# Performance work log

Measured on AMD Instinct MI355X. Metric: run time of the kernel, lower is better.

The kernel has to match this reference:

```python
import jax, jax.numpy as jnp
import numpy as np

N_NODES = 100000
N_EDGES = 1600000
IN_DIM, HID_DIM, OUT_DIM = 128, 64, 32


def gcn_conv(x, edge_index, W, b, n_nodes):
    """PyG GCNConv: add self-loops, symmetric deg^-1/2 normalization,
    linear transform, gather->scatter-sum aggregation, then bias."""
    loops = jnp.arange(n_nodes, dtype=edge_index.dtype)
    src = jnp.concatenate([edge_index[0], loops])  # [E+N]
    dst = jnp.concatenate([edge_index[1], loops])  # [E+N]
    # degree over targets (includes self-loops)
    deg = jax.ops.segment_sum(jnp.ones_like(dst, dtype=x.dtype), dst,
                              num_segments=n_nodes)
    dinv = jnp.where(deg > 0, jax.lax.rsqrt(deg), 0.0)
    norm = dinv[src] * dinv[dst]                   # [E+N]
    h = x @ W                                      # [N, F_out]
    msg = h[src] * norm[:, None]                   # gather + scale
    out = jax.ops.segment_sum(msg, dst, num_segments=n_nodes)
    return out + b


def setup_inputs() -> dict:
    key = jax.random.key(0)
    k1, k2, k3, k4 = jax.random.split(key, 4)
    x = jax.random.normal(k1, (N_NODES, IN_DIM), dtype=jnp.float32)
    edge_index = jax.random.randint(k2, (2, N_EDGES), 0, N_NODES,
                                    dtype=jnp.int64)
    # Glorot-ish init for weights, zero bias (PyG default: glorot + zeros)
    W1 = jax.random.normal(k3, (IN_DIM, HID_DIM), dtype=jnp.float32) * (1.0 / np.sqrt(IN_DIM))
    b1 = jnp.zeros((HID_DIM,), dtype=jnp.float32)
    W2 = jax.random.normal(k4, (HID_DIM, OUT_DIM), dtype=jnp.float32) * (1.0 / np.sqrt(HID_DIM))
    b2 = jnp.zeros((OUT_DIM,), dtype=jnp.float32)
    return {"x": x, "edge_index": edge_index, "W1": W1, "b1": b1,
            "W2": W2, "b2": b2}


def reference(x, edge_index, W1, b1, W2, b2):
    n = x.shape[0]
    h = jax.nn.relu(gcn_conv(x, edge_index, W1, b1, n))
    return gcn_conv(h, edge_index, W2, b2, n)
```

## Files before the change

kernel.cpp:

```cpp
#include <hip/hip_runtime.h>


#define BLK 256
#define BLKC 1024
#define EPT 8
#define BSHIFT 10
#define NPB 1024
#define SLOTB 18432
#define NBMAX 128

typedef unsigned int uint_t;
typedef unsigned short ushort_t;
typedef __attribute__((ext_vector_type(2))) float v2f;
typedef __attribute__((ext_vector_type(8))) short bf16x8;
typedef __attribute__((ext_vector_type(4))) float f32x4;

__device__ __forceinline__ uint_t f2bf(float x) {
    union { float f; uint_t u; } un; un.f = x;
    uint_t u = un.u;
    return (u + 0x7fffu + ((u >> 16) & 1u)) >> 16;
}

__device__ __forceinline__ void pkadd(v2f& a0, v2f& a1, v2f& a2, v2f& a3, uint4 v) {
    v2f p;
    p.x = __uint_as_float(v.x << 16); p.y = __uint_as_float(v.x & 0xffff0000u); a0 += p;
    p.x = __uint_as_float(v.y << 16); p.y = __uint_as_float(v.y & 0xffff0000u); a1 += p;
    p.x = __uint_as_float(v.z << 16); p.y = __uint_as_float(v.z & 0xffff0000u); a2 += p;
    p.x = __uint_as_float(v.w << 16); p.y = __uint_as_float(v.w & 0xffff0000u); a3 += p;
}

__device__ __forceinline__ bool detect64(const int* __restrict__ idx) {
    int z = 0;
#pragma unroll
    for (int i = 1; i < 32; i += 2) z |= idx[i];
    return z == 0;
}

__global__ void k_part(const int* __restrict__ idx, int* __restrict__ bcursor,
                       int* __restrict__ edge_part, int E, int nbuck) {
    __shared__ int h[NBMAX];
    __shared__ int rb[NBMAX];
    bool is64 = detect64(idx);
    int t = threadIdx.x, blk = blockIdx.x;
    for (int i = t; i < nbuck; i += BLK) h[i] = 0;
    __syncthreads();
    int base = blk * (BLK * EPT) + t;
    int dst[EPT], src[EPT];
#pragma unroll
    for (int k = 0; k < EPT; ++k) {
        int e = base + k * BLK;
        if (e < E) {
            if (is64) {
                uint2 dv = ((const uint2*)idx)[(size_t)E + e];
                uint2 sv = ((const uint2*)idx)[e];
                dst[k] = (int)dv.x;
                src[k] = (int)sv.x;
            } else {
                dst[k] = idx[E + e];
                src[k] = idx[e];
            }
            atomicAdd(&h[dst[k] >> BSHIFT], 1);
        } else {
            dst[k] = -1;
        }
    }
    __syncthreads();
    for (int i = t; i < nbuck; i += BLK) {
        int c = h[i];
        rb[i] = c ? atomicAdd(&bcursor[i], c) : 0;
        h[i] = 0;
    }
    __syncthreads();
#pragma unroll
    for (int k = 0; k < EPT; ++k) {
        if (dst[k] >= 0) {
            int b = dst[k] >> BSHIFT;
            int r = atomicAdd(&h[b], 1);
            edge_part[(size_t)b * SLOTB + rb[b] + r] =
                src[k] | ((dst[k] & (NPB - 1)) << 17);
        }
    }
}

__global__ __launch_bounds__(BLKC) void k_csr(
        const int* __restrict__ edge_part, const int* __restrict__ bcursor,
        int* __restrict__ row_ptr, int* __restrict__ deg, float* __restrict__ dinv,
        int* __restrict__ csr_src, int N, int nbuck) {
    __shared__ int cnt[NPB];
    __shared__ int off[NPB];
    int b = blockIdx.x, t = threadIdx.x;
    int node0 = b << BSHIFT;
    int nn = min(NPB, N - node0);
    int m = bcursor[b];
    size_t ebase = (size_t)b * SLOTB;
    cnt[t] = 0;
    __syncthreads();
    for (int e = t; e < m; e += BLKC)
        atomicAdd(&cnt[((unsigned)edge_part[ebase + e]) >> 17], 1);
    __syncthreads();
    off[t] = cnt[t];
    __syncthreads();
    for (int st = 1; st < BLKC; st <<= 1) {
        int v = (t >= st) ? off[t - st] : 0;
        __syncthreads();
        off[t] += v;
        __syncthreads();
    }
    int excl = off[t] - cnt[t];
    off[t] = excl;
    if (t < nn) {
        row_ptr[node0 + t] = (int)(ebase + excl);
        deg[node0 + t] = cnt[t];
        dinv[node0 + t] = rsqrtf((float)(cnt[t] + 1));
    }
    __syncthreads();
    for (int e = t; e < m; e += BLKC) {
        int p = edge_part[ebase + e];
        int dlo = ((unsigned)p) >> 17;
        int r = atomicAdd(&off[dlo], 1);
        csr_src[ebase + r] = p & 0x1FFFF;
    }
}

__global__ __launch_bounds__(256) void k_gemm1(
        const float* __restrict__ x, const float* __restrict__ W1,
        const float* __restrict__ dinv, ushort_t* __restrict__ hs1, int N) {
    __shared__ ushort_t xb[64][136];
    __shared__ ushort_t wb[64][136];
    int t = threadIdx.x;
    int rbase = blockIdx.x * 64;
    for (int i = t; i < 2048; i += BLK) {
        int k = i >> 4, n4 = i & 15;
        float4 w = ((const float4*)W1)[i];
        wb[4 * n4 + 0][k] = (ushort_t)f2bf(w.x);
        wb[4 * n4 + 1][k] = (ushort_t)f2bf(w.y);
        wb[4 * n4 + 2][k] = (ushort_t)f2bf(w.z);
        wb[4 * n4 + 3][k] = (ushort_t)f2bf(w.w);
    }
    for (int i = t; i < 2048; i += BLK) {
        int r = i >> 5, c4 = i & 31;
        int rr = rbase + r; if (rr >= N) rr = N - 1;
        float4 v = ((const float4*)x)[(size_t)rr * 32 + c4];
        uint2 p;
        p.x = f2bf(v.x) | (f2bf(v.y) << 16);
        p.y = f2bf(v.z) | (f2bf(v.w) << 16);
        *(uint2*)&xb[r][4 * c4] = p;
    }
    __syncthreads();
    int w = t >> 6, l = t & 63;
    int lane16 = l & 15, quad = l >> 4;
    int mrow = 16 * w + lane16;
    f32x4 acc0 = {0.f, 0.f, 0.f, 0.f}, acc1 = {0.f, 0.f, 0.f, 0.f};
    f32x4 acc2 = {0.f, 0.f, 0.f, 0.f}, acc3 = {0.f, 0.f, 0.f, 0.f};
#pragma unroll
    for (int kk = 0; kk < 4; ++kk) {
        int k0 = kk * 32 + quad * 8;
        bf16x8 a  = *(const bf16x8*)&xb[mrow][k0];
        bf16x8 b0 = *(const bf16x8*)&wb[lane16][k0];
        bf16x8 b1 = *(const bf16x8*)&wb[lane16 + 16][k0];
        bf16x8 b2 = *(const bf16x8*)&wb[lane16 + 32][k0];
        bf16x8 b3 = *(const bf16x8*)&wb[lane16 + 48][k0];
        acc0 = __builtin_amdgcn_mfma_f32_16x16x32_bf16(a, b0, acc0, 0, 0, 0);
        acc1 = __builtin_amdgcn_mfma_f32_16x16x32_bf16(a, b1, acc1, 0, 0, 0);
        acc2 = __builtin_amdgcn_mfma_f32_16x16x32_bf16(a, b2, acc2, 0, 0, 0);
        acc3 = __builtin_amdgcn_mfma_f32_16x16x32_bf16(a, b3, acc3, 0, 0, 0);
    }
    __syncthreads();
    int orow = 16 * w + quad * 4;
    float d0 = dinv[min(rbase + orow + 0, N - 1)];
    float d1 = dinv[min(rbase + orow + 1, N - 1)];
    float d2 = dinv[min(rbase + orow + 2, N - 1)];
    float d3 = dinv[min(rbase + orow + 3, N - 1)];
    xb[orow + 0][lane16]      = (ushort_t)f2bf(acc0.x * d0);
    xb[orow + 1][lane16]      = (ushort_t)f2bf(acc0.y * d1);
    xb[orow + 2][lane16]      = (ushort_t)f2bf(acc0.z * d2);
    xb[orow + 3][lane16]      = (ushort_t)f2bf(acc0.w * d3);
    xb[orow + 0][lane16 + 16] = (ushort_t)f2bf(acc1.x * d0);
    xb[orow + 1][lane16 + 16] = (ushort_t)f2bf(acc1.y * d1);
    xb[orow + 2][lane16 + 16] = (ushort_t)f2bf(acc1.z * d2);
    xb[orow + 3][lane16 + 16] = (ushort_t)f2bf(acc1.w * d3);
    xb[orow + 0][lane16 + 32] = (ushort_t)f2bf(acc2.x * d0);
    xb[orow + 1][lane16 + 32] = (ushort_t)f2bf(acc2.y * d1);
    xb[orow + 2][lane16 + 32] = (ushort_t)f2bf(acc2.z * d2);
    xb[orow + 3][lane16 + 32] = (ushort_t)f2bf(acc2.w * d3);
    xb[orow + 0][lane16 + 48] = (ushort_t)f2bf(acc3.x * d0);
    xb[orow + 1][lane16 + 48] = (ushort_t)f2bf(acc3.y * d1);
    xb[orow + 2][lane16 + 48] = (ushort_t)f2bf(acc3.z * d2);
    xb[orow + 3][lane16 + 48] = (ushort_t)f2bf(acc3.w * d3);
    __syncthreads();
    for (int i = t; i < 512; i += BLK) {
        int r = i >> 3, c8 = i & 7;
        int rr = rbase + r;
        if (rr < N) {
            uint4 v = *(const uint4*)&xb[r][8 * c8];
            *(uint4*)&hs1[(size_t)rr * 64 + 8 * c8] = v;
        }
    }
}

__global__ void k_agg1(const uint_t* __restrict__ hs1, const int* __restrict__ row_ptr,
                       const int* __restrict__ deg, const int* __restrict__ csr_src,
                       const float* __restrict__ dinv, const float* __restrict__ b1,
                       ushort_t* __restrict__ a1b, int N) {
    int lane = threadIdx.x & 63;
    int g = lane >> 3;
    int c = lane & 7;
    int wavebase = ((blockIdx.x * blockDim.x + threadIdx.x) >> 6) * 8;
    int node = wavebase + g;
    bool alive = node < N;
    int nodeC = alive ? node : N - 1;
    const uint4* H = (const uint4*)hs1;
    v2f a0 = {0.f, 0.f}, a1_ = {0.f, 0.f}, a2 = {0.f, 0.f}, a3 = {0.f, 0.f};
    float dn = dinv[nodeC];
    int beg = row_ptr[nodeC];
    int tot = alive ? deg[nodeC] : 0;
    pkadd(a0, a1_, a2, a3, H[(size_t)nodeC * 8 + c]);
    int gbase = lane & 0x38;
    for (int eb = 0; __any(eb < tot); eb += 8) {
        int jal = 0;
        if (eb + c < tot) jal = csr_src[beg + eb + c];
        int cnt = tot - eb;
        uint4 vv[8];
#pragma unroll
        for (int e = 0; e < 8; ++e) {
            int j = __shfl(jal, gbase + e, 64);
            if (e < cnt) vv[e] = H[(size_t)j * 8 + c];
        }
#pragma unroll
        for (int e = 0; e < 8; ++e) {
            if (e < cnt) pkadd(a0, a1_, a2, a3, vv[e]);
        }
    }
    if (alive) {
        const float4* B = (const float4*)b1;
        float4 bv0 = B[2 * c], bv1 = B[2 * c + 1];
        float o0 = fmaxf(fmaf(a0.x, dn, bv0.x), 0.f);
        float o1 = fmaxf(fmaf(a0.y, dn, bv0.y), 0.f);
        float o2 = fmaxf(fmaf(a1_.x, dn, bv0.z), 0.f);
        float o3 = fmaxf(fmaf(a1_.y, dn, bv0.w), 0.f);
        float o4 = fmaxf(fmaf(a2.x, dn, bv1.x), 0.f);
        float o5 = fmaxf(fmaf(a2.y, dn, bv1.y), 0.f);
        float o6 = fmaxf(fmaf(a3.x, dn, bv1.z), 0.f);
        float o7 = fmaxf(fmaf(a3.y, dn, bv1.w), 0.f);
        uint4 o;
        o.x = f2bf(o0) | (f2bf(o1) << 16);
        o.y = f2bf(o2) | (f2bf(o3) << 16);
        o.z = f2bf(o4) | (f2bf(o5) << 16);
        o.w = f2bf(o6) | (f2bf(o7) << 16);
        ((uint4*)a1b)[(size_t)node * 8 + c] = o;
    }
}

__global__ __launch_bounds__(256) void k_gemm2(
        const ushort_t* __restrict__ a1b, const float* __restrict__ W2,
        const float* __restrict__ dinv, ushort_t* __restrict__ hs2, int N) {
    __shared__ ushort_t ab[64][72];
    __shared__ ushort_t wb[32][72];
    int t = threadIdx.x;
    int rbase = blockIdx.x * 64;
    for (int i = t; i < 512; i += BLK) {
        int k = i >> 3, n4 = i & 7;
        float4 w = ((const float4*)W2)[i];
        wb[4 * n4 + 0][k] = (ushort_t)f2bf(w.x);
        wb[4 * n4 + 1][k] = (ushort_t)f2bf(w.y);
        wb[4 * n4 + 2][k] = (ushort_t)f2bf(w.z);
        wb[4 * n4 + 3][k] = (ushort_t)f2bf(w.w);
    }
    for (int i = t; i < 512; i += BLK) {
        int r = i >> 3, c8 = i & 7;
        int rr = rbase + r; if (rr >= N) rr = N - 1;
        uint4 v = ((const uint4*)a1b)[(size_t)rr * 8 + c8];
        *(uint4*)&ab[r][8 * c8] = v;
    }
    __syncthreads();
    int w = t >> 6, l = t & 63;
    int lane16 = l & 15, quad = l >> 4;
    int mrow = 16 * w + lane16;
    f32x4 acc0 = {0.f, 0.f, 0.f, 0.f}, acc1 = {0.f, 0.f, 0.f, 0.f};
#pragma unroll
    for (int kk = 0; kk < 2; ++kk) {
        int k0 = kk * 32 + quad * 8;
        bf16x8 a  = *(const bf16x8*)&ab[mrow][k0];
        bf16x8 b0 = *(const bf16x8*)&wb[lane16][k0];
        bf16x8 b1 = *(const bf16x8*)&wb[lane16 + 16][k0];
        acc0 = __builtin_amdgcn_mfma_f32_16x16x32_bf16(a, b0, acc0, 0, 0, 0);
        acc1 = __builtin_amdgcn_mfma_f32_16x16x32_bf16(a, b1, acc1, 0, 0, 0);
    }
    __syncthreads();
    int orow = 16 * w + quad * 4;
    float d0 = dinv[min(rbase + orow + 0, N - 1)];
    float d1 = dinv[min(rbase + orow + 1, N - 1)];
    float d2 = dinv[min(rbase + orow + 2, N - 1)];
    float d3 = dinv[min(rbase + orow + 3, N - 1)];
    ab[orow + 0][lane16]      = (ushort_t)f2bf(acc0.x * d0);
    ab[orow + 1][lane16]      = (ushort_t)f2bf(acc0.y * d1);
    ab[orow + 2][lane16]      = (ushort_t)f2bf(acc0.z * d2);
    ab[orow + 3][lane16]      = (ushort_t)f2bf(acc0.w * d3);
    ab[orow + 0][lane16 + 16] = (ushort_t)f2bf(acc1.x * d0);
    ab[orow + 1][lane16 + 16] = (ushort_t)f2bf(acc1.y * d1);
    ab[orow + 2][lane16 + 16] = (ushort_t)f2bf(acc1.z * d2);
    ab[orow + 3][lane16 + 16] = (ushort_t)f2bf(acc1.w * d3);
    __syncthreads();
    for (int i = t; i < 256; i += BLK) {
        int r = i >> 2, c4 = i & 3;
        int rr = rbase + r;
        if (rr < N) {
            uint4 v = *(const uint4*)&ab[r][8 * c4];
            *(uint4*)&hs2[(size_t)rr * 32 + 8 * c4] = v;
        }
    }
}

__global__ void k_agg2(const uint_t* __restrict__ hs2, const int* __restrict__ row_ptr,
                       const int* __restrict__ deg, const int* __restrict__ csr_src,
                       const float* __restrict__ dinv, const float* __restrict__ b2,
                       float* __restrict__ out, int N) {
    int lane = threadIdx.x & 63;
    int g = lane >> 2;
    int c = lane & 3;
    int wavebase = ((blockIdx.x * blockDim.x + threadIdx.x) >> 6) * 16;
    int node = wavebase + g;
    bool alive = node < N;
    int nodeC = alive ? node : N - 1;
    const uint4* H = (const uint4*)hs2;
    v2f a0 = {0.f, 0.f}, a1_ = {0.f, 0.f}, a2 = {0.f, 0.f}, a3 = {0.f, 0.f};
    float dn = dinv[nodeC];
    int beg = row_ptr[nodeC];
    int tot = alive ? deg[nodeC] : 0;
    pkadd(a0, a1_, a2, a3, H[(size_t)nodeC * 4 + c]);
    int gbase = lane & 0x3C;
    for (int eb = 0; __any(eb < tot); eb += 4) {
        int jal = 0;
        if (eb + c < tot) jal = csr_src[beg + eb + c];
        int cnt = tot - eb;
        uint4 vv[4];
#pragma unroll
        for (int e = 0; e < 4; ++e) {
            int j = __shfl(jal, gbase + e, 64);
            if (e < cnt) vv[e] = H[(size_t)j * 4 + c];
        }
#pragma unroll
        for (int e = 0; e < 4; ++e) {
            if (e < cnt) pkadd(a0, a1_, a2, a3, vv[e]);
        }
    }
    if (alive) {
        const float4* B = (const float4*)b2;
        float4 bv0 = B[2 * c], bv1 = B[2 * c + 1];
        float4 o0, o1;
        o0.x = fmaf(a0.x, dn, bv0.x);
        o0.y = fmaf(a0.y, dn, bv0.y);
        o0.z = fmaf(a1_.x, dn, bv0.z);
        o0.w = fmaf(a1_.y, dn, bv0.w);
        o1.x = fmaf(a2.x, dn, bv1.x);
        o1.y = fmaf(a2.y, dn, bv1.y);
        o1.z = fmaf(a3.x, dn, bv1.z);
        o1.w = fmaf(a3.y, dn, bv1.w);
        float4* O = (float4*)out;
        O[(size_t)node * 8 + 2 * c] = o0;
        O[(size_t)node * 8 + 2 * c + 1] = o1;
    }
}

extern "C" void kernel_launch(void* const* d_in, const int* in_sizes, int n_in,
                              void* d_out, int out_size, void* d_ws, size_t ws_size,
                              hipStream_t stream) {
    const float* x  = (const float*)d_in[0];
    const int*   idx = (const int*)d_in[1];
    const float* W1 = (const float*)d_in[2];
    const float* b1 = (const float*)d_in[3];
    const float* W2 = (const float*)d_in[4];
    const float* b2 = (const float*)d_in[5];
    float* out = (float*)d_out;

    const int N = in_sizes[0] / 128;
    const int E = in_sizes[1] / 2;
    const int nbuck = (N + NPB - 1) >> BSHIFT;
    const int PB = (E + BLK * EPT - 1) / (BLK * EPT);

    char* ws = (char*)d_ws;
    size_t off = 0;
    auto alloc = [&](size_t bytes) -> char* {
        char* p = ws + off;
        off = (off + bytes + 255) & ~(size_t)255;
        return p;
    };
    float* dinv     = (float*)alloc((size_t)N * 4);
    int*   row_ptr  = (int*)alloc((size_t)N * 4);
    int*   deg      = (int*)alloc((size_t)N * 4);
    int*   bcursor  = (int*)alloc((size_t)nbuck * 4);
    int*   csr_src  = (int*)alloc((size_t)nbuck * SLOTB * 4);
    size_t ep_bytes = (size_t)nbuck * SLOTB * 4;
    size_t h1_bytes = (size_t)N * 64 * 2;
    int*   edge_part = (int*)alloc(ep_bytes > h1_bytes ? ep_bytes : h1_bytes);
    ushort_t* a1b   = (ushort_t*)alloc((size_t)N * 64 * 2);
    ushort_t* hs1   = (ushort_t*)edge_part;
    ushort_t* hs2   = hs1;

    hipMemsetAsync(bcursor, 0, (size_t)nbuck * 4, stream);
    k_part<<<PB, BLK, 0, stream>>>(idx, bcursor, edge_part, E, nbuck);
    k_csr<<<nbuck, BLKC, 0, stream>>>(edge_part, bcursor, row_ptr, deg, dinv,
                                      csr_src, N, nbuck);
    k_gemm1<<<(N + 63) / 64, BLK, 0, stream>>>(x, W1, dinv, hs1, N);
    k_agg1<<<(N * 8 + BLK - 1) / BLK, BLK, 0, stream>>>(
        (const uint_t*)hs1, row_ptr, deg, csr_src, dinv, b1, a1b, N);
    k_gemm2<<<(N + 63) / 64, BLK, 0, stream>>>(a1b, W2, dinv, hs2, N);
    k_agg2<<<(N * 4 + BLK - 1) / BLK, BLK, 0, stream>>>(
        (const uint_t*)hs2, row_ptr, deg, csr_src, dinv, b2, out, N);
}
```

Baseline: 220.8 us.

## Double-buffer neighbor gathers in aggregation and reuse atomic ranks in partition/CSR

The aggregation kernels now compute a wave-wide chunk count and software-pipeline the neighbor feature gathers with two register buffers, so loads for the next chunk are in flight while the current one is accumulated. The partition and CSR kernels keep the rank returned by the first shared-memory atomic and reuse it for the scatter, which drops the second atomic pass and the re-read of edge_part. This costs more registers, which may lower occupancy. The CSR kernel also caps each bucket at CITER×BLKC edges (18432), matching SLOTB.

```diff
diff --git a/kernel.cpp b/kernel.cpp
--- a/kernel.cpp
+++ b/kernel.cpp
@@ -4,6 +4,7 @@
 #define BLK 256
 #define BLKC 1024
 #define EPT 8
+#define CITER 18
 #define BSHIFT 10
 #define NPB 1024
 #define SLOTB 18432
@@ -45,7 +46,7 @@
     for (int i = t; i < nbuck; i += BLK) h[i] = 0;
     __syncthreads();
     int base = blk * (BLK * EPT) + t;
-    int dst[EPT], src[EPT];
+    int dst[EPT], src[EPT], rk[EPT];
 #pragma unroll
     for (int k = 0; k < EPT; ++k) {
         int e = base + k * BLK;
@@ -59,7 +60,7 @@
                 dst[k] = idx[E + e];
                 src[k] = idx[e];
             }
-            atomicAdd(&h[dst[k] >> BSHIFT], 1);
+            rk[k] = atomicAdd(&h[dst[k] >> BSHIFT], 1);
         } else {
             dst[k] = -1;
         }
@@ -68,15 +69,13 @@
     for (int i = t; i < nbuck; i += BLK) {
         int c = h[i];
         rb[i] = c ? atomicAdd(&bcursor[i], c) : 0;
-        h[i] = 0;
     }
     __syncthreads();
 #pragma unroll
     for (int k = 0; k < EPT; ++k) {
         if (dst[k] >= 0) {
             int b = dst[k] >> BSHIFT;
-            int r = atomicAdd(&h[b], 1);
-            edge_part[(size_t)b * SLOTB + rb[b] + r] =
+            edge_part[(size_t)b * SLOTB + rb[b] + rk[k]] =
                 src[k] | ((dst[k] & (NPB - 1)) << 17);
         }
     }
@@ -95,8 +94,16 @@
     size_t ebase = (size_t)b * SLOTB;
     cnt[t] = 0;
     __syncthreads();
-    for (int e = t; e < m; e += BLKC)
-        atomicAdd(&cnt[((unsigned)edge_part[ebase + e]) >> 17], 1);
+    int pp[CITER], rr[CITER];
+#pragma unroll
+    for (int it = 0; it < CITER; ++it) {
+        int e = t + it * BLKC;
+        if (e < m) {
+            int p = edge_part[ebase + e];
+            pp[it] = p;
+            rr[it] = atomicAdd(&cnt[((unsigned)p) >> 17], 1);
+        }
+    }
     __syncthreads();
     off[t] = cnt[t];
     __syncthreads();
@@ -114,11 +121,14 @@
         dinv[node0 + t] = rsqrtf((float)(cnt[t] + 1));
     }
     __syncthreads();
-    for (int e = t; e < m; e += BLKC) {
-        int p = edge_part[ebase + e];
-        int dlo = ((unsigned)p) >> 17;
-        int r = atomicAdd(&off[dlo], 1);
-        csr_src[ebase + r] = p & 0x1FFFF;
+#pragma unroll
+    for (int it = 0; it < CITER; ++it) {
+        int e = t + it * BLKC;
+        if (e < m) {
+            int p = pp[it];
+            int dlo = ((unsigned)p) >> 17;
+            csr_src[ebase + off[dlo] + rr[it]] = p & 0x1FFFF;
+        }
     }
 }
 
@@ -210,27 +220,44 @@
     bool alive = node < N;
     int nodeC = alive ? node : N - 1;
     const uint4* H = (const uint4*)hs1;
-    v2f a0 = {0.f, 0.f}, a1_ = {0.f, 0.f}, a2 = {0.f, 0.f}, a3 = {0.f, 0.f};
     float dn = dinv[nodeC];
     int beg = row_ptr[nodeC];
     int tot = alive ? deg[nodeC] : 0;
-    pkadd(a0, a1_, a2, a3, H[(size_t)nodeC * 8 + c]);
+    uint4 selfv = H[(size_t)nodeC * 8 + c];
     int gbase = lane & 0x38;
-    for (int eb = 0; __any(eb < tot); eb += 8) {
-        int jal = 0;
-        if (eb + c < tot) jal = csr_src[beg + eb + c];
-        int cnt = tot - eb;
-        uint4 vv[8];
+    int wtot = tot;
+    wtot = max(wtot, __shfl_xor(wtot, 8, 64));
+    wtot = max(wtot, __shfl_xor(wtot, 16, 64));
+    wtot = max(wtot, __shfl_xor(wtot, 32, 64));
+    int nch = (wtot + 7) >> 3;
+    v2f a0 = {0.f, 0.f}, a1_ = {0.f, 0.f}, a2 = {0.f, 0.f}, a3 = {0.f, 0.f};
+    uint4 vA[8], vB[8];
+    auto ISSUE = [&](uint4 (&vv)[8], int i) {
+        int base = 8 * i;
+        int jal = (base + c < tot) ? csr_src[beg + base + c] : 0;
 #pragma unroll
         for (int e = 0; e < 8; ++e) {
             int j = __shfl(jal, gbase + e, 64);
-            if (e < cnt) vv[e] = H[(size_t)j * 8 + c];
-        }
-#pragma unroll
-        for (int e = 0; e < 8; ++e) {
-            if (e < cnt) pkadd(a0, a1_, a2, a3, vv[e]);
-        }
-    }
+            if (base + e < tot) vv[e] = H[(size_t)j * 8 + c];
+        }
+    };
+    auto CONSUME = [&](uint4 (&vv)[8], int i) {
+        int base = 8 * i;
+#pragma unroll
+        for (int e = 0; e < 8; ++e)
+            if (base + e < tot) pkadd(a0, a1_, a2, a3, vv[e]);
+    };
+    if (nch > 0) {
+        ISSUE(vA, 0);
+        int i = 1;
+        for (; i + 1 < nch; i += 2) {
+            ISSUE(vB, i);     CONSUME(vA, i - 1);
+            ISSUE(vA, i + 1); CONSUME(vB, i);
+        }
+        if (i < nch) { ISSUE(vB, i); CONSUME(vA, i - 1); CONSUME(vB, i); }
+        else          CONSUME(vA, i - 1);
+    }
+    pkadd(a0, a1_, a2, a3, selfv);
     if (alive) {
         const float4* B = (const float4*)b1;
         float4 bv0 = B[2 * c], bv1 = B[2 * c + 1];
@@ -323,27 +350,45 @@
     bool alive = node < N;
     int nodeC = alive ? node : N - 1;
     const uint4* H = (const uint4*)hs2;
-    v2f a0 = {0.f, 0.f}, a1_ = {0.f, 0.f}, a2 = {0.f, 0.f}, a3 = {0.f, 0.f};
     float dn = dinv[nodeC];
     int beg = row_ptr[nodeC];
     int tot = alive ? deg[nodeC] : 0;
-    pkadd(a0, a1_, a2, a3, H[(size_t)nodeC * 4 + c]);
+    uint4 selfv = H[(size_t)nodeC * 4 + c];
     int gbase = lane & 0x3C;
-    for (int eb = 0; __any(eb < tot); eb += 4) {
-        int jal = 0;
-        if (eb + c < tot) jal = csr_src[beg + eb + c];
-        int cnt = tot - eb;
-        uint4 vv[4];
+    int wtot = tot;
+    wtot = max(wtot, __shfl_xor(wtot, 4, 64));
+    wtot = max(wtot, __shfl_xor(wtot, 8, 64));
+    wtot = max(wtot, __shfl_xor(wtot, 16, 64));
+    wtot = max(wtot, __shfl_xor(wtot, 32, 64));
+    int nch = (wtot + 3) >> 2;
+    v2f a0 = {0.f, 0.f}, a1_ = {0.f, 0.f}, a2 = {0.f, 0.f}, a3 = {0.f, 0.f};
+    uint4 vA[4], vB[4];
+    auto ISSUE = [&](uint4 (&vv)[4], int i) {
+        int base = 4 * i;
+        int jal = (base + c < tot) ? csr_src[beg + base + c] : 0;
 #pragma unroll
         for (int e = 0; e < 4; ++e) {
             int j = __shfl(jal, gbase + e, 64);
-            if (e < cnt) vv[e] = H[(size_t)j * 4 + c];
-        }
-#pragma unroll
-        for (int e = 0; e < 4; ++e) {
-            if (e < cnt) pkadd(a0, a1_, a2, a3, vv[e]);
-        }
-    }
+            if (base + e < tot) vv[e] = H[(size_t)j * 4 + c];
+        }
+    };
+    auto CONSUME = [&](uint4 (&vv)[4], int i) {
+        int base = 4 * i;
+#pragma unroll
+        for (int e = 0; e < 4; ++e)
+            if (base + e < tot) pkadd(a0, a1_, a2, a3, vv[e]);
+    };
+    if (nch > 0) {
+        ISSUE(vA, 0);
+        int i = 1;
+        for (; i + 1 < nch; i += 2) {
+            ISSUE(vB, i);     CONSUME(vA, i - 1);
+            ISSUE(vA, i + 1); CONSUME(vB, i);
+        }
+        if (i < nch) { ISSUE(vB, i); CONSUME(vA, i - 1); CONSUME(vB, i); }
+        else          CONSUME(vA, i - 1);
+    }
+    pkadd(a0, a1_, a2, a3, selfv);
     if (alive) {
         const float4* B = (const float4*)b2;
         float4 bv0 = B[2 * c], bv1 = B[2 * c + 1];
```

After: 220.4 us. Within noise of the previous version (-0.2%).
